# Performance work log

Measured on AMD Instinct MI355X. Metric: run time of the kernel, lower is better.

Reference implementation:

```python
import jax, jax.numpy as jnp
import numpy as np

B, T, N_EMBD, HEAD_SIZE = 8, 2048, 1024, 128

def setup_inputs() -> dict:
    key = jax.random.key(0)
    kx, kk, kq, kv = jax.random.split(key, 4)
    scale = 1.0 / np.sqrt(N_EMBD)
    return {
        "x": jax.random.normal(kx, (B, T, N_EMBD), dtype=jnp.float32),
        "Wk": jax.random.normal(kk, (N_EMBD, HEAD_SIZE), dtype=jnp.float32) * scale,
        "Wq": jax.random.normal(kq, (N_EMBD, HEAD_SIZE), dtype=jnp.float32) * scale,
        "Wv": jax.random.normal(kv, (N_EMBD, HEAD_SIZE), dtype=jnp.float32) * scale,
    }

def reference(x, Wk, Wq, Wv):
    # x: [B, T, C]; projections: [C, H]
    k = jnp.einsum("btc,ch->bth", x, Wk)
    q = jnp.einsum("btc,ch->bth", x, Wq)
    v = jnp.einsum("btc,ch->bth", x, Wv)
    # NOTE: original code does tf.divide(scores, 1/sqrt(n_embd)) == scores * sqrt(n_embd)
    wei = jnp.einsum("bqh,bkh->bqk", q, k) * jnp.sqrt(jnp.float32(N_EMBD))  # [B, T, T]
    # causal mask via band_part (zero out upper triangle) then zeros -> -inf, as in source
    tril = jnp.tril(wei)
    wei = jnp.where(tril == 0.0, -jnp.inf, tril)
    wei = jax.nn.softmax(wei, axis=-1)
    out = jnp.einsum("bqk,bkh->bqh", wei, v)  # [B, T, H]
    return out
```

## Files before the change

kernel.cpp:

```cpp
#include <hip/hip_runtime.h>
#include <hip/hip_bf16.h>

typedef float  f32x4  __attribute__((ext_vector_type(4)));
typedef __bf16 bf16x8 __attribute__((ext_vector_type(8)));
typedef unsigned int   u32;
typedef unsigned short u16;
typedef u32   u32x2  __attribute__((ext_vector_type(2)));
typedef u32   u32x4  __attribute__((ext_vector_type(4)));
typedef u16   u16x4  __attribute__((ext_vector_type(4)));
typedef u16   u16x8  __attribute__((ext_vector_type(8)));

#define DEV __device__ __forceinline__

constexpr int NB = 8, T = 2048, C = 1024, H = 128;
constexpr int BT = NB * T;

union Frag {
  bf16x8 v;
  u32x4  u4;
  u32x2  u2[2];
  u32    u[4];
  u16    s[8];
};

DEV u16 f2bu(float f) {
  __hip_bfloat16 h = __float2bfloat16(f);
  return __builtin_bit_cast(u16, h);
}
DEV float bu2f(u16 u) {
  return __bfloat162float(__builtin_bit_cast(__hip_bfloat16, u));
}
DEV f32x4 MFMA(bf16x8 a, bf16x8 b, f32x4 c) {
  return __builtin_amdgcn_mfma_f32_16x16x32_bf16(a, b, c, 0, 0, 0);
}


__global__ void prep_w(const float* __restrict__ Wk, const float* __restrict__ Wq,
                       const float* __restrict__ Wv,
                       u16* __restrict__ wpq, u16* __restrict__ wpk,
                       u16* __restrict__ wpv) {
  const int id = blockIdx.x * 256 + threadIdx.x;
  if (id >= 24 * 32 * 64) return;
  const int lane = id & 63;
  const int kc   = (id >> 6) & 31;
  const int tile = id >> 11;
  const int mat  = tile >> 3;
  const int tt   = tile & 7;
  const int n    = tt * 16 + (lane & 15);
  const float* W = (mat == 0) ? Wq : (mat == 1) ? Wk : Wv;
  u16x8 hi, lo;
  #pragma unroll
  for (int e = 0; e < 8; ++e) {
    const int k = kc * 32 + 4 * (lane >> 4) + (e & 3) + 16 * (e >> 2);
    const float w = W[(size_t)k * H + n];
    u16 h = f2bu(w);
    hi[e] = h;
    lo[e] = f2bu(w - bu2f(h));
  }
  if (mat == 2) {
    *(u16x8*)(wpv + ((size_t)(tt * 32 + kc) * 64 + lane) * 8) = hi;
  } else {
    u16* p = ((mat == 0) ? wpq : wpk) +
             (((size_t)(tt * 32 + kc) * 2 + 0) * 64 + lane) * 8;
    *(u16x8*)p         = hi;
    *(u16x8*)(p + 512) = lo;
  }
}

__global__ __launch_bounds__(256, 2) void proj_kernel(
    const float* __restrict__ x,
    const u16* __restrict__ wpq, const u16* __restrict__ wpk,
    const u16* __restrict__ wpv,
    u16* __restrict__ qpk, u16* __restrict__ kpk, u16* __restrict__ vpk) {
  __shared__ u16 xh[2][128][36];
  __shared__ u16 xl[2][128][36];
  __shared__ u16 wsl[2][640 * 8];
  const int tid  = threadIdx.x;
  const int ng   = blockIdx.x >> 7;
  const int mt   = blockIdx.x & 127;
  const int m0   = mt * 128;
  const int w    = tid >> 6;
  const int lane = tid & 63;
  const int lg   = lane >> 4, lc = lane & 15;

  const u16* wbase[3];
  int wstep[3], wofs[3];
  bool wact[3];
  #pragma unroll
  for (int i = 0; i < 3; ++i) {
    const int c = tid + 256 * i;
    wact[i] = (c < 640);
    const int cc = wact[i] ? c : 0;
    const int p  = cc >> 6;
    const int ln = cc & 63;
    const u16* base;
    int stride;
    if (p < 4) {
      base = wpq + (size_t)((2 * ng + (p >> 1)) * 32) * 1024 + (p & 1) * 512 + ln * 8;
      stride = 1024;
    } else if (p < 8) {
      base = wpk + (size_t)((2 * ng + ((p - 4) >> 1)) * 32) * 1024 + ((p - 4) & 1) * 512 + ln * 8;
      stride = 1024;
    } else {
      base = wpv + (size_t)((2 * ng + (p - 8)) * 32) * 512 + ln * 8;
      stride = 512;
    }
    wbase[i] = base;
    wstep[i] = stride;
    wofs[i]  = (p * 64 + ln) * 8;
  }

  f32x4 zero = {0.f, 0.f, 0.f, 0.f};
  f32x4 acc[6][2];
  #pragma unroll
  for (int j = 0; j < 6; ++j)
    #pragma unroll
    for (int s = 0; s < 2; ++s) acc[j][s] = zero;

  f32x4 xreg[4];
  u16x8 wreg[3];

  auto loadX = [&](int ks) {
    const int k = ks > 31 ? 31 : ks;
    #pragma unroll
    for (int j = 0; j < 4; ++j) {
      const int idx = tid + 256 * j;
      const int row = idx >> 3;
      const int c4  = (idx & 7) * 4;
      xreg[j] = *(const f32x4*)&x[(size_t)(m0 + row) * C + k * 32 + c4];
    }
  };
  auto writeX = [&](int buf) {
    #pragma unroll
    for (int j = 0; j < 4; ++j) {
      const int idx = tid + 256 * j;
      const int row = idx >> 3;
      const int c4  = (idx & 7) * 4;
      u16x4 hv, lv;
      #pragma unroll
      for (int e = 0; e < 4; ++e) {
        u16 h = f2bu(xreg[j][e]);
        hv[e] = h;
        lv[e] = f2bu(xreg[j][e] - bu2f(h));
      }
      *(u16x4*)&xh[buf][row][c4] = hv;
      *(u16x4*)&xl[buf][row][c4] = lv;
    }
  };
  auto loadW = [&](int ks) {
    const int k = ks > 31 ? 31 : ks;
    #pragma unroll
    for (int i = 0; i < 3; ++i)
      if (wact[i]) wreg[i] = *(const u16x8*)(wbase[i] + (size_t)k * wstep[i]);
  };
  auto writeW = [&](int buf) {
    #pragma unroll
    for (int i = 0; i < 3; ++i)
      if (wact[i]) *(u16x8*)&wsl[buf][wofs[i]] = wreg[i];
  };

  auto compute = [&](int buf) {
    Frag axh[2], axl[2];
    #pragma unroll
    for (int s = 0; s < 2; ++s) {
      const int row = 32 * w + 16 * s + lc;
      axh[s].u2[0] = *(const u32x2*)&xh[buf][row][4 * lg];
      axh[s].u2[1] = *(const u32x2*)&xh[buf][row][16 + 4 * lg];
      axl[s].u2[0] = *(const u32x2*)&xl[buf][row][4 * lg];
      axl[s].u2[1] = *(const u32x2*)&xl[buf][row][16 + 4 * lg];
    }
    #pragma unroll
    for (int jt = 0; jt < 2; ++jt) {
      Frag qh, ql, kh, kl, vh;
      qh.u4 = *(const u32x4*)&wsl[buf][((0 + jt * 2 + 0) * 64 + lane) * 8];
      ql.u4 = *(const u32x4*)&wsl[buf][((0 + jt * 2 + 1) * 64 + lane) * 8];
      kh.u4 = *(const u32x4*)&wsl[buf][((4 + jt * 2 + 0) * 64 + lane) * 8];
      kl.u4 = *(const u32x4*)&wsl[buf][((4 + jt * 2 + 1) * 64 + lane) * 8];
      vh.u4 = *(const u32x4*)&wsl[buf][((8 + jt) * 64 + lane) * 8];
      #pragma unroll
      for (int s = 0; s < 2; ++s) {
        acc[jt][s]     = MFMA(axh[s].v, qh.v, acc[jt][s]);
        acc[jt][s]     = MFMA(axh[s].v, ql.v, acc[jt][s]);
        acc[jt][s]     = MFMA(axl[s].v, qh.v, acc[jt][s]);
        acc[2 + jt][s] = MFMA(axh[s].v, kh.v, acc[2 + jt][s]);
        acc[2 + jt][s] = MFMA(axh[s].v, kl.v, acc[2 + jt][s]);
        acc[2 + jt][s] = MFMA(axl[s].v, kh.v, acc[2 + jt][s]);
        acc[4 + jt][s] = MFMA(axh[s].v, vh.v, acc[4 + jt][s]);
      }
    }
  };

  loadX(0); loadW(0);
  writeX(0); writeW(0);
  loadX(1); loadW(1);
  __syncthreads();
  int cur = 0;
  for (int ks = 0; ks < 32; ++ks) {
    writeX(cur ^ 1);
    writeW(cur ^ 1);
    loadX(ks + 2);
    loadW(ks + 2);
    compute(cur);
    __syncthreads();
    cur ^= 1;
  }

  #pragma unroll
  for (int s = 0; s < 2; ++s) {
    const int tb_abs = mt * 8 + 2 * w + s;
    const int b  = tb_abs >> 7;
    const int tb = tb_abs & 127;
    #pragma unroll
    for (int j = 0; j < 6; ++j) {
      const int mat = j >> 1;
      const int jt  = j & 1;
      const int tt  = 2 * ng + jt;
      #pragma unroll
      for (int r = 0; r < 4; ++r) {
        const float val = acc[j][s][r];
        if (mat < 2) {
          const u16 hvv = f2bu(val);
          const u16 lvv = f2bu(val - bu2f(hvv));
          const int lane_c = 4 * lg + r + 16 * (lc >> 2);
          const int hs = tt >> 1;
          const int e  = (lc & 3) + 4 * (tt & 1);
          u16* dst = ((mat == 0) ? qpk : kpk) +
                     (((size_t)(b * 128 + tb) * 4 + hs) * 2 * 64 + lane_c) * 8 + e;
          dst[0]   = hvv;
          dst[512] = lvv;
        } else {
          const int kt = tb >> 1;
          const int lane_c = lc + 16 * lg;
          const int e = r + 4 * (tb & 1);
          vpk[(((size_t)(b * 64 + kt) * 8 + tt) * 64 + lane_c) * 8 + e] = f2bu(val);
        }
      }
    }
  }
}

__global__ __launch_bounds__(512, 4) void attn_kernel(
    const u16* __restrict__ qpk, const u16* __restrict__ kpk,
    const u16* __restrict__ vpk, float* __restrict__ out) {
  __shared__ float lm[8][16];
  __shared__ float ll[8][16];
  __shared__ u16 lo[8][16][132];

  const int bid = blockIdx.x;
  const int b   = bid & 7;
  const int qt  = bid >> 3;
  const int w    = threadIdx.x >> 6;
  const int lane = threadIdx.x & 63;
  const int lg = lane >> 4, lc = lane & 15;

  Frag bqh[4], bql[4];
  const u16* qp = qpk + (size_t)(b * 128 + qt) * 4096 + lane * 8;
  #pragma unroll
  for (int hs = 0; hs < 4; ++hs) {
    bqh[hs].u4 = *(const u32x4*)(qp + (size_t)(hs * 2 + 0) * 512);
    bql[hs].u4 = *(const u32x4*)(qp + (size_t)(hs * 2 + 1) * 512);
  }

  f32x4 zero = {0.f, 0.f, 0.f, 0.f};
  f32x4 o_acc[8];
  #pragma unroll
  for (int i = 0; i < 8; ++i) o_acc[i] = zero;
  float m_run = -INFINITY, l_run = 0.f;

  const int myq = qt * 16 + lc;
  const int nkb = qt >> 2;

  for (int kb = w; kb <= nkb; kb += 8) {
    f32x4 s[4];
    #pragma unroll
    for (int t = 0; t < 4; ++t) s[t] = zero;

    const u16* kp = kpk + (size_t)(b * 128 + kb * 4) * 4096 + lane * 8;
    __builtin_amdgcn_s_setprio(1);
    #pragma unroll
    for (int t = 0; t < 4; ++t) {
      #pragma unroll
      for (int hs = 0; hs < 4; ++hs) {
        const u16* p = kp + (size_t)(t * 8 + hs * 2) * 512;
        Frag akh, akl;
        akh.u4 = *(const u32x4*)p;
        akl.u4 = *(const u32x4*)(p + 512);
        s[t] = MFMA(akh.v, bqh[hs].v, s[t]);
        s[t] = MFMA(akh.v, bql[hs].v, s[t]);
        s[t] = MFMA(akl.v, bqh[hs].v, s[t]);
      }
    }
    __builtin_amdgcn_s_setprio(0);

    float pmax = -INFINITY;
    #pragma unroll
    for (int t = 0; t < 4; ++t) {
      #pragma unroll
      for (int r = 0; r < 4; ++r) {
        const int kk = kb * 64 + t * 16 + 4 * lg + r;
        float v = s[t][r] * 32.0f;
        if (kk > myq || v == 0.0f) v = -INFINITY;
        s[t][r] = v;
        pmax = fmaxf(pmax, v);
      }
    }
    pmax = fmaxf(pmax, __shfl_xor(pmax, 16));
    pmax = fmaxf(pmax, __shfl_xor(pmax, 32));
    const float m_new = fmaxf(m_run, pmax);
    const float alpha = __expf(m_run - m_new);

    float sum = 0.f;
    u16 pb[16];
    #pragma unroll
    for (int t = 0; t < 4; ++t) {
      #pragma unroll
      for (int r = 0; r < 4; ++r) {
        const float p = __expf(s[t][r] - m_new);
        sum += p;
        pb[t * 4 + r] = f2bu(p);
      }
    }
    sum += __shfl_xor(sum, 16);
    sum += __shfl_xor(sum, 32);
    l_run = l_run * alpha + sum;
    m_run = m_new;

    float al[4];
    #pragma unroll
    for (int r = 0; r < 4; ++r) al[r] = __shfl(alpha, 4 * lg + r);
    #pragma unroll
    for (int i = 0; i < 8; ++i) {
      #pragma unroll
      for (int r = 0; r < 4; ++r) o_acc[i][r] *= al[r];
    }

    Frag pa[2];
    #pragma unroll
    for (int ks = 0; ks < 2; ++ks) {
      #pragma unroll
      for (int e = 0; e < 8; ++e)
        pa[ks].s[e] = pb[(2 * ks + (e >> 2)) * 4 + (e & 3)];
    }

    __builtin_amdgcn_s_setprio(1);
    #pragma unroll
    for (int ks = 0; ks < 2; ++ks) {
      const u16* vp = vpk + (size_t)(b * 64 + kb * 2 + ks) * 4096 + lane * 8;
      #pragma unroll
      for (int ht = 0; ht < 8; ++ht) {
        Frag bv;
        bv.u4 = *(const u32x4*)(vp + (size_t)ht * 512);
        o_acc[ht] = MFMA(pa[ks].v, bv.v, o_acc[ht]);
      }
    }
    __builtin_amdgcn_s_setprio(0);
  }

  if (lane < 16) { lm[w][lane] = m_run; ll[w][lane] = l_run; }
  #pragma unroll
  for (int ht = 0; ht < 8; ++ht)
    #pragma unroll
    for (int r = 0; r < 4; ++r)
      lo[w][4 * lg + r][ht * 16 + lc] = f2bu(o_acc[ht][r]);
  __syncthreads();

  const int tid = threadIdx.x;
  const int q  = tid >> 5;
  const int hb = (tid & 31) * 4;
  float M = -INFINITY;
  #pragma unroll
  for (int ww = 0; ww < 8; ++ww) M = fmaxf(M, lm[ww][q]);
  float lsum = 0.f;
  f32x4 osum = {0.f, 0.f, 0.f, 0.f};
  #pragma unroll
  for (int ww = 0; ww < 8; ++ww) {
    const float sc = __expf(lm[ww][q] - M);
    lsum += sc * ll[ww][q];
    const u16x4 ov = *(const u16x4*)&lo[ww][q][hb];
    #pragma unroll
    for (int j = 0; j < 4; ++j) osum[j] += sc * bu2f(ov[j]);
  }
  const float inv = 1.0f / lsum;
  f32x4 res = {osum[0] * inv, osum[1] * inv, osum[2] * inv, osum[3] * inv};
  *(f32x4*)&out[((size_t)(b * T + qt * 16 + q)) * H + hb] = res;
}

extern "C" void kernel_launch(void* const* d_in, const int* in_sizes, int n_in,
                              void* d_out, int out_size, void* d_ws, size_t ws_size,
                              hipStream_t stream) {
  (void)in_sizes; (void)n_in; (void)out_size; (void)ws_size;
  const float* x  = (const float*)d_in[0];
  const float* Wk = (const float*)d_in[1];
  const float* Wq = (const float*)d_in[2];
  const float* Wv = (const float*)d_in[3];
  float* out = (float*)d_out;

  u16* w = (u16*)d_ws;
  const size_t WPQK = (size_t)8 * 32 * 2 * 64 * 8;
  const size_t WPV  = (size_t)8 * 32 * 64 * 8;
  const size_t QKP  = (size_t)NB * 128 * 4 * 2 * 64 * 8;
  u16* wpq = w;
  u16* wpk = wpq + WPQK;
  u16* wpv = wpk + WPQK;
  u16* qpk = wpv + WPV;
  u16* kpk = qpk + QKP;
  u16* vpk = kpk + QKP;

  prep_w<<<192, 256, 0, stream>>>(Wk, Wq, Wv, wpq, wpk, wpv);
  proj_kernel<<<512, 256, 0, stream>>>(x, wpq, wpk, wpv, qpk, kpk, vpk);
  attn_kernel<<<NB * (T / 16), 512, 0, stream>>>(qpk, kpk, vpk, out);
}
```

Baseline: 97.74 us.

## Load packed projection weights directly from global instead of staging in LDS

The projection kernel no longer stages the pre-packed Wq/Wk/Wv fragments through a double-buffered LDS array. Each wave now reads its MFMA B-fragments straight from global memory at the current k-step. This removes the LDS writes and reads for the weights and frees about 20KB of shared memory, and the launch bound is raised to 4 blocks per CU to take advantage of the lower footprint. In exchange, every wave issues its own global loads for the same weight tiles, with no prefetch ahead of the MFMAs, so load latency may be exposed and cache traffic goes up.

```diff
diff --git a/kernel.cpp b/kernel.cpp
--- a/kernel.cpp
+++ b/kernel.cpp
@@ -67,14 +67,13 @@
   }
 }
 
-__global__ __launch_bounds__(256, 2) void proj_kernel(
+__global__ __launch_bounds__(256, 4) void proj_kernel(
     const float* __restrict__ x,
     const u16* __restrict__ wpq, const u16* __restrict__ wpk,
     const u16* __restrict__ wpv,
     u16* __restrict__ qpk, u16* __restrict__ kpk, u16* __restrict__ vpk) {
   __shared__ u16 xh[2][128][36];
   __shared__ u16 xl[2][128][36];
-  __shared__ u16 wsl[2][640 * 8];
   const int tid  = threadIdx.x;
   const int ng   = blockIdx.x >> 7;
   const int mt   = blockIdx.x & 127;
@@ -83,31 +82,14 @@
   const int lane = tid & 63;
   const int lg   = lane >> 4, lc = lane & 15;
 
-  const u16* wbase[3];
-  int wstep[3], wofs[3];
-  bool wact[3];
-  #pragma unroll
-  for (int i = 0; i < 3; ++i) {
-    const int c = tid + 256 * i;
-    wact[i] = (c < 640);
-    const int cc = wact[i] ? c : 0;
-    const int p  = cc >> 6;
-    const int ln = cc & 63;
-    const u16* base;
-    int stride;
-    if (p < 4) {
-      base = wpq + (size_t)((2 * ng + (p >> 1)) * 32) * 1024 + (p & 1) * 512 + ln * 8;
-      stride = 1024;
-    } else if (p < 8) {
-      base = wpk + (size_t)((2 * ng + ((p - 4) >> 1)) * 32) * 1024 + ((p - 4) & 1) * 512 + ln * 8;
-      stride = 1024;
-    } else {
-      base = wpv + (size_t)((2 * ng + (p - 8)) * 32) * 512 + ln * 8;
-      stride = 512;
-    }
-    wbase[i] = base;
-    wstep[i] = stride;
-    wofs[i]  = (p * 64 + ln) * 8;
+  const u16* wq_b[2];
+  const u16* wk_b[2];
+  const u16* wv_b[2];
+  #pragma unroll
+  for (int jt = 0; jt < 2; ++jt) {
+    wq_b[jt] = wpq + (size_t)((2 * ng + jt) * 32) * 1024 + lane * 8;
+    wk_b[jt] = wpk + (size_t)((2 * ng + jt) * 32) * 1024 + lane * 8;
+    wv_b[jt] = wpv + (size_t)((2 * ng + jt) * 32) * 512 + lane * 8;
   }
 
   f32x4 zero = {0.f, 0.f, 0.f, 0.f};
@@ -118,7 +100,6 @@
     for (int s = 0; s < 2; ++s) acc[j][s] = zero;
 
   f32x4 xreg[4];
-  u16x8 wreg[3];
 
   auto loadX = [&](int ks) {
     const int k = ks > 31 ? 31 : ks;
@@ -147,19 +128,8 @@
       *(u16x4*)&xl[buf][row][c4] = lv;
     }
   };
-  auto loadW = [&](int ks) {
-    const int k = ks > 31 ? 31 : ks;
-    #pragma unroll
-    for (int i = 0; i < 3; ++i)
-      if (wact[i]) wreg[i] = *(const u16x8*)(wbase[i] + (size_t)k * wstep[i]);
-  };
-  auto writeW = [&](int buf) {
-    #pragma unroll
-    for (int i = 0; i < 3; ++i)
-      if (wact[i]) *(u16x8*)&wsl[buf][wofs[i]] = wreg[i];
-  };
-
-  auto compute = [&](int buf) {
+
+  auto compute = [&](int buf, int ks) {
     Frag axh[2], axl[2];
     #pragma unroll
     for (int s = 0; s < 2; ++s) {
@@ -172,11 +142,11 @@
     #pragma unroll
     for (int jt = 0; jt < 2; ++jt) {
       Frag qh, ql, kh, kl, vh;
-      qh.u4 = *(const u32x4*)&wsl[buf][((0 + jt * 2 + 0) * 64 + lane) * 8];
-      ql.u4 = *(const u32x4*)&wsl[buf][((0 + jt * 2 + 1) * 64 + lane) * 8];
-      kh.u4 = *(const u32x4*)&wsl[buf][((4 + jt * 2 + 0) * 64 + lane) * 8];
-      kl.u4 = *(const u32x4*)&wsl[buf][((4 + jt * 2 + 1) * 64 + lane) * 8];
-      vh.u4 = *(const u32x4*)&wsl[buf][((8 + jt) * 64 + lane) * 8];
+      qh.u4 = *(const u32x4*)(wq_b[jt] + (size_t)ks * 1024);
+      ql.u4 = *(const u32x4*)(wq_b[jt] + (size_t)ks * 1024 + 512);
+      kh.u4 = *(const u32x4*)(wk_b[jt] + (size_t)ks * 1024);
+      kl.u4 = *(const u32x4*)(wk_b[jt] + (size_t)ks * 1024 + 512);
+      vh.u4 = *(const u32x4*)(wv_b[jt] + (size_t)ks * 512);
       #pragma unroll
       for (int s = 0; s < 2; ++s) {
         acc[jt][s]     = MFMA(axh[s].v, qh.v, acc[jt][s]);
@@ -190,17 +160,15 @@
     }
   };
 
-  loadX(0); loadW(0);
-  writeX(0); writeW(0);
-  loadX(1); loadW(1);
+  loadX(0);
+  writeX(0);
+  loadX(1);
   __syncthreads();
   int cur = 0;
   for (int ks = 0; ks < 32; ++ks) {
     writeX(cur ^ 1);
-    writeW(cur ^ 1);
     loadX(ks + 2);
-    loadW(ks + 2);
-    compute(cur);
+    compute(cur, ks);
     __syncthreads();
     cur ^= 1;
   }
```

After: 119.9 us. +22.6%, slower.
